# Performance work log

Measured on AMD Instinct MI355X. Metric: run time of the kernel, lower is better.

Reference implementation:

```python
import jax, jax.numpy as jnp
import numpy as np
import math

B, S, D, H = 2, 2048, 512, 8
DK = D // H  # 64
NEG_INF = float('-inf')


def setup_inputs() -> dict:
    key = jax.random.key(0)
    ks = jax.random.split(key, 16)
    s = 1.0 / math.sqrt(D)
    return {
        'in_Q': jax.random.normal(ks[0], (B, S, D), jnp.float32),
        'in_K': jax.random.normal(ks[1], (B, S, D), jnp.float32),
        'in_V': jax.random.normal(ks[2], (B, S, D), jnp.float32),
        'row_pad_mask': jax.random.randint(ks[3], (B, S), 0, 2, jnp.int32),
        'col_pad_mask': jax.random.randint(ks[4], (B, S), 0, 2, jnp.int32),
        'W_Q': jax.random.uniform(ks[5], (D, D), jnp.float32, -s, s),
        'b_Q': jax.random.uniform(ks[6], (D,), jnp.float32, -s, s),
        'W_K': jax.random.uniform(ks[7], (D, D), jnp.float32, -s, s),
        'b_K': jax.random.uniform(ks[8], (D,), jnp.float32, -s, s),
        'W_V': jax.random.uniform(ks[9], (D, D), jnp.float32, -s, s),
        'b_V': jax.random.uniform(ks[10], (D,), jnp.float32, -s, s),
        'W_O': jax.random.uniform(ks[11], (D, D), jnp.float32, -s, s),
        'b_O': jax.random.uniform(ks[12], (D,), jnp.float32, -s, s),
    }


def reference(in_Q, in_K, in_V, row_pad_mask, col_pad_mask,
              W_Q, b_Q, W_K, b_K, W_V, b_V, W_O, b_O):
    b, sq, _ = in_Q.shape
    sk = in_K.shape[1]
    # projections (torch Linear: x @ W.T + b)
    Q = in_Q @ W_Q.T + b_Q
    K = in_K @ W_K.T + b_K
    V = in_V @ W_V.T + b_V
    # chunk along feature dim + stack == reshape to heads: [b, h, s, dk]
    Qh = Q.reshape(b, sq, H, DK).transpose(0, 2, 1, 3)
    Kh = K.reshape(b, sk, H, DK).transpose(0, 2, 1, 3)
    Vh = V.reshape(b, sk, H, DK).transpose(0, 2, 1, 3)
    scores = jnp.einsum('bhqd,bhkd->bhqk', Qh, Kh) / math.sqrt(DK)
    # causal mask (additive -inf above diagonal, as in the original)
    causal = jnp.triu(jnp.full((sq, sk), NEG_INF, scores.dtype), k=1)
    scores = scores + causal
    # padding masks: pad masks encode lengths via their row sums
    row_len = row_pad_mask.sum(axis=1)  # [b]
    col_len = col_pad_mask.sum(axis=1)
    row_np = jnp.arange(sq)[None, :] < row_len[:, None]  # [b, sq]
    col_np = jnp.arange(sk)[None, :] < col_len[:, None]  # [b, sk]
    non_pad = (row_np[:, :, None] & col_np[:, None, :])[:, None]  # [b,1,sq,sk]
    scores = jnp.where(non_pad, scores, NEG_INF)
    p = jax.nn.softmax(scores, axis=-1)
    p = jnp.nan_to_num(p)  # fully-masked rows -> 0 (matches torch nan_to_num)
    attn = jnp.einsum('bhqk,bhkd->bhqd', p, Vh)
    Hcat = attn.transpose(0, 2, 1, 3).reshape(b, sq, D)
    return Hcat @ W_O.T + b_O
```

## Files before the change

kernel.cpp:

```cpp
#include <hip/hip_runtime.h>

#define S_LEN 2048
#define D_MODEL 512
#define NHEAD 8
#define BATCH 2

typedef __attribute__((ext_vector_type(8))) short bf16x8;
typedef __attribute__((ext_vector_type(4))) float f32x4;

__device__ __forceinline__ unsigned short f2bf(float f) {
    union { float f; unsigned u; } v; v.f = f;
    unsigned u = v.u + 0x7FFFu + ((v.u >> 16) & 1u);
    return (unsigned short)(u >> 16);
}

__device__ __forceinline__ void gl_lds16(const unsigned short* g, unsigned short* l) {
    __builtin_amdgcn_global_load_lds(
        (const __attribute__((address_space(1))) void*)g,
        (__attribute__((address_space(3))) void*)l,
        16, 0, 0);
}

__global__ __launch_bounds__(256) void cvtlens_kernel(
    const float* __restrict__ inQ, const float* __restrict__ inK, const float* __restrict__ inV,
    const float* __restrict__ WQ, const float* __restrict__ WK,
    const float* __restrict__ WV, const float* __restrict__ WO,
    const int* __restrict__ rpm, const int* __restrict__ cpm,
    unsigned short* __restrict__ Xbf, unsigned short* __restrict__ Wbf,
    int* __restrict__ lens)
{
    const int t = threadIdx.x;
    if (blockIdx.x < 2) {
        __shared__ int red[256];
        const int b = blockIdx.x;
        int sr = 0, sc2 = 0;
        for (int i = t; i < S_LEN; i += 256) {
            sr  += rpm[b * S_LEN + i];
            sc2 += cpm[b * S_LEN + i];
        }
        red[t] = sr;
        __syncthreads();
        for (int off = 128; off > 0; off >>= 1) {
            if (t < off) red[t] += red[t + off];
            __syncthreads();
        }
        if (t == 0) lens[b * 2 + 0] = red[0];
        __syncthreads();
        red[t] = sc2;
        __syncthreads();
        for (int off = 128; off > 0; off >>= 1) {
            if (t < off) red[t] += red[t + off];
            __syncthreads();
        }
        if (t == 0) lens[b * 2 + 1] = red[0];
    }

    const int NXC = 786432;
    const int NTOT = 917504;
    const int stride = gridDim.x * 256;
    for (int c = blockIdx.x * 256 + t; c < NTOT; c += stride) {
        if (c < NXC) {
            const int flat = c << 3;
            const int z = flat >> 21;
            const int off = flat & 2097151;
            const float* src = ((z == 0) ? inQ : (z == 1) ? inK : inV) + off;
            float4 a = *(const float4*)src;
            float4 d = *(const float4*)(src + 4);
            unsigned short* w = Xbf + flat;
            w[0] = f2bf(a.x); w[1] = f2bf(a.y); w[2] = f2bf(a.z); w[3] = f2bf(a.w);
            w[4] = f2bf(d.x); w[5] = f2bf(d.y); w[6] = f2bf(d.z); w[7] = f2bf(d.w);
        } else {
            const int wflat = (c - NXC) << 3;
            const int wz = wflat >> 18;
            const int off = wflat & 262143;
            const float* src = ((wz == 0) ? WQ : (wz == 1) ? WK : (wz == 2) ? WV : WO) + off;
            float4 a = *(const float4*)src;
            float4 d = *(const float4*)(src + 4);
            unsigned short* w = Wbf + wflat;
            w[0] = f2bf(a.x); w[1] = f2bf(a.y); w[2] = f2bf(a.z); w[3] = f2bf(a.w);
            w[4] = f2bf(d.x); w[5] = f2bf(d.y); w[6] = f2bf(d.z); w[7] = f2bf(d.w);
        }
    }
}

__global__ __launch_bounds__(256) void proj_gemm(
    const unsigned short* __restrict__ Xbf, const unsigned short* __restrict__ Wbf,
    const float* __restrict__ bQ, const float* __restrict__ bK, const float* __restrict__ bV,
    const int* __restrict__ lens,
    unsigned short* __restrict__ Qg, unsigned short* __restrict__ Kg,
    unsigned short* __restrict__ VTg)
{
    __shared__ __align__(16) unsigned short Xld[2][8192];
    __shared__ __align__(16) unsigned short Wld[2][8192];

    const int z = blockIdx.z;
    const int tileS = blockIdx.x * 128;
    const int tileF = blockIdx.y * 128;
    const int bb0 = tileS >> 11;
    const int rl = lens[bb0 * 2], cl = lens[bb0 * 2 + 1];
    const int limit = (z == 0) ? rl : cl;
    if ((tileS & 2047) >= limit) return;

    const unsigned short* X = Xbf + (size_t)z * (4096 * 512);
    const unsigned short* W = Wbf + (size_t)z * (512 * 512);
    const float* bias = (z == 0) ? bQ : (z == 1) ? bK : bV;

    const int t = threadIdx.x;
    const int wv = t >> 6, lane = t & 63, l15 = lane & 15, quad = lane >> 4;
    const int ro = lane >> 3;
    const int lc8 = ((lane & 7) ^ ro) * 8;

    const unsigned short* gX = X + (size_t)(tileS + wv * 32 + ro) * 512 + lc8;
    const unsigned short* gW = W + (size_t)(tileF + wv * 32 + ro) * 512 + lc8;
    const int wvo = wv * 2048;

    const int f_off = (wv & 1) * 64, s_off = (wv >> 1) * 64;
    const int swk = l15 & 7;

    f32x4 acc[4][4] = {};

    #pragma unroll
    for (int j = 0; j < 4; ++j) {
        gl_lds16(gX + j * 4096, &Xld[0][wvo + j * 512]);
        gl_lds16(gW + j * 4096, &Wld[0][wvo + j * 512]);
    }

    for (int kk = 0; kk < 8; ++kk) {
        __syncthreads();
        if (kk < 7) {
            const int k0 = (kk + 1) * 64;
            const int nb = (kk + 1) & 1;
            #pragma unroll
            for (int j = 0; j < 4; ++j) {
                gl_lds16(gX + k0 + j * 4096, &Xld[nb][wvo + j * 512]);
                gl_lds16(gW + k0 + j * 4096, &Wld[nb][wvo + j * 512]);
            }
        }
        const unsigned short* Xb = Xld[kk & 1];
        const unsigned short* Wb = Wld[kk & 1];
        #pragma unroll
        for (int kk2 = 0; kk2 < 2; ++kk2) {
            bf16x8 wf[4], xf[4];
            #pragma unroll
            for (int i = 0; i < 4; ++i) {
                const int rw = f_off + i * 16 + l15;
                wf[i] = *(const bf16x8*)(Wb + rw * 64 + ((kk2 * 4 + quad) ^ swk) * 8);
                const int rx = s_off + i * 16 + l15;
                xf[i] = *(const bf16x8*)(Xb + rx * 64 + ((kk2 * 4 + quad) ^ swk) * 8);
            }
            #pragma unroll
            for (int ft = 0; ft < 4; ++ft)
                #pragma unroll
                for (int st = 0; st < 4; ++st)
                    acc[ft][st] = __builtin_amdgcn_mfma_f32_16x16x32_bf16(
                        wf[ft], xf[st], acc[ft][st], 0, 0, 0);
        }
    }

    const float oscale = (z == 0) ? 0.125f : 1.0f;
    #pragma unroll
    for (int ft = 0; ft < 4; ++ft) {
        const int f = tileF + f_off + ft * 16 + quad * 4;
        const int h = f >> 6, dk = f & 63;
        const float b0 = bias[f], b1 = bias[f + 1], b2 = bias[f + 2], b3 = bias[f + 3];
        #pragma unroll
        for (int st = 0; st < 4; ++st) {
            const int s = tileS + s_off + st * 16 + l15;
            const int bb = s >> 11, seq = s & 2047;
            const f32x4 a = acc[ft][st];
            if (z <= 1) {
                unsigned short* dst = ((z == 0) ? Qg : Kg)
                    + ((size_t)((bb * 8 + h) * 2048 + seq)) * 64 + dk;
                ushort4 u;
                u.x = f2bf((a[0] + b0) * oscale); u.y = f2bf((a[1] + b1) * oscale);
                u.z = f2bf((a[2] + b2) * oscale); u.w = f2bf((a[3] + b3) * oscale);
                *(ushort4*)dst = u;
            } else {
                unsigned short* dst = VTg
                    + ((size_t)((bb * 8 + h) * 64 + dk)) * 2048 + seq;
                dst[0]    = f2bf(a[0] + b0);
                dst[2048] = f2bf(a[1] + b1);
                dst[4096] = f2bf(a[2] + b2);
                dst[6144] = f2bf(a[3] + b3);
            }
        }
    }
}

__global__ __launch_bounds__(256) void attn_kernel(
    const unsigned short* __restrict__ Qg, const unsigned short* __restrict__ Kg,
    const unsigned short* __restrict__ VTg, const int* __restrict__ lens,
    unsigned short* __restrict__ AO)
{
    __shared__ __align__(16) char smem[32768 + 9216 + 512];
    unsigned short* stage = (unsigned short*)smem;
    unsigned short* Plb   = (unsigned short*)(smem + 32768);
    float* Ml = (float*)(smem + 32768 + 9216);
    float* Ll = Ml + 64;

    const int t = threadIdx.x;
    const int wv = t >> 6, lane = t & 63, l15 = lane & 15, quad = lane >> 4;
    const int bh = blockIdx.y;
    const int b = bh >> 3, h = bh & 7;
    const int q0 = blockIdx.x * 16;
    const int rl = lens[b * 2], cl = lens[b * 2 + 1];

    if (q0 >= rl) {
        const int row = t >> 4, cg = t & 15;
        ushort4 zz = {0, 0, 0, 0};
        *(ushort4*)(AO + ((size_t)(b * 2048 + q0 + row)) * 512 + h * 64 + cg * 4) = zz;
        return;
    }

    const unsigned short* Qrow = Qg + ((size_t)(bh * 2048 + q0 + l15)) * 64;
    const bf16x8 aq0 = *(const bf16x8*)(Qrow + quad * 8);
    const bf16x8 aq1 = *(const bf16x8*)(Qrow + 32 + quad * 8);

    unsigned short* stw = stage + wv * 4096;
    unsigned short* pb  = Plb + wv * (16 * 72);

    const int sro = lane >> 3;
    const int sc8 = ((lane & 7) ^ sro) * 8;
    const int kg_off  = sro * 64 + sc8;
    const int vtg_off = sro * 2048 + sc8;
    const int sw7 = l15 & 7;

    f32x4 oacc[4] = {};
    float m_[4], l_[4];
    #pragma unroll
    for (int r = 0; r < 4; ++r) { m_[r] = -__builtin_inff(); l_[r] = 0.f; }

    const int q_end = q0 + 16;
    const int kv_max = (cl < q_end) ? cl : q_end;
    const int ntiles = (kv_max + 63) >> 6;
    const int qrow0 = q0 + quad * 4;

    for (int kt = wv; kt < ntiles; kt += 4) {
        const int kv0 = kt * 64;

        {
            const unsigned short* kg = Kg + ((size_t)(bh * 2048 + kv0)) * 64 + kg_off;
            #pragma unroll
            for (int j = 0; j < 8; ++j)
                gl_lds16(kg + j * 512, stw + j * 512);
        }
        __builtin_amdgcn_s_waitcnt(0x0070);

        f32x4 sc[4] = {};
        #pragma unroll
        for (int ct = 0; ct < 4; ++ct) {
            const unsigned short* krow = stw + (ct * 16 + l15) * 64;
            const bf16x8 kf0 = *(const bf16x8*)(krow + ((quad    ) ^ sw7) * 8);
            const bf16x8 kf1 = *(const bf16x8*)(krow + ((quad + 4) ^ sw7) * 8);
            sc[ct] = __builtin_amdgcn_mfma_f32_16x16x32_bf16(aq0, kf0, sc[ct], 0, 0, 0);
            sc[ct] = __builtin_amdgcn_mfma_f32_16x16x32_bf16(aq1, kf1, sc[ct], 0, 0, 0);
        }
        __builtin_amdgcn_s_waitcnt(0x0070);

        {
            const unsigned short* vg = VTg + ((size_t)(bh * 64)) * 2048 + kv0 + vtg_off;
            #pragma unroll
            for (int j = 0; j < 8; ++j)
                gl_lds16(vg + j * 16384, stw + j * 512);
        }

        const bool full = (kv0 + 64 <= q0) && (kv0 + 64 <= cl) && (q_end <= rl);

        #pragma unroll
        for (int r = 0; r < 4; ++r) {
            const int q = qrow0 + r;
            float mx = -__builtin_inff();
            if (full) {
                #pragma unroll
                for (int ct = 0; ct < 4; ++ct) mx = fmaxf(mx, sc[ct][r]);
            } else {
                #pragma unroll
                for (int ct = 0; ct < 4; ++ct) {
                    const int kv = kv0 + ct * 16 + l15;
                    float s = sc[ct][r];
                    const bool valid = (q < rl) && (kv < cl) && (kv <= q);
                    s = valid ? s : -__builtin_inff();
                    sc[ct][r] = s;
                    mx = fmaxf(mx, s);
                }
            }
            mx = fmaxf(mx, __shfl_xor(mx, 1, 16));
            mx = fmaxf(mx, __shfl_xor(mx, 2, 16));
            mx = fmaxf(mx, __shfl_xor(mx, 4, 16));
            mx = fmaxf(mx, __shfl_xor(mx, 8, 16));

            const float mold = m_[r];
            const float mnew = fmaxf(mold, mx);
            const float alpha = (mold == -__builtin_inff()) ? 0.f : __expf(mold - mnew);
            float psum = 0.f;
            #pragma unroll
            for (int ct = 0; ct < 4; ct++) {
                const float sv = sc[ct][r];
                const float p = (mnew == -__builtin_inff()) ? 0.f : __expf(sv - mnew);
                sc[ct][r] = p;
                psum += p;
            }
            psum += __shfl_xor(psum, 1, 16);
            psum += __shfl_xor(psum, 2, 16);
            psum += __shfl_xor(psum, 4, 16);
            psum += __shfl_xor(psum, 8, 16);
            l_[r] = alpha * l_[r] + psum;
            m_[r] = mnew;
            #pragma unroll
            for (int ct = 0; ct < 4; ct++) oacc[ct][r] *= alpha;
        }

        #pragma unroll
        for (int ct = 0; ct < 4; ++ct) {
            #pragma unroll
            for (int r = 0; r < 4; ++r)
                pb[(quad * 4 + r) * 72 + ct * 16 + l15] = f2bf(sc[ct][r]);
        }
        const bf16x8 pf0 = *(const bf16x8*)(pb + l15 * 72 + quad * 8);
        const bf16x8 pf1 = *(const bf16x8*)(pb + l15 * 72 + 32 + quad * 8);

        __builtin_amdgcn_s_waitcnt(0x0070);
        #pragma unroll
        for (int ct = 0; ct < 4; ++ct) {
            const unsigned short* vrow = stw + (ct * 16 + l15) * 64;
            const bf16x8 vf0 = *(const bf16x8*)(vrow + ((quad    ) ^ sw7) * 8);
            const bf16x8 vf1 = *(const bf16x8*)(vrow + ((quad + 4) ^ sw7) * 8);
            oacc[ct] = __builtin_amdgcn_mfma_f32_16x16x32_bf16(pf0, vf0, oacc[ct], 0, 0, 0);
            oacc[ct] = __builtin_amdgcn_mfma_f32_16x16x32_bf16(pf1, vf1, oacc[ct], 0, 0, 0);
        }
    }

    if (l15 == 0) {
        #pragma unroll
        for (int r = 0; r < 4; ++r) {
            Ml[wv * 16 + quad * 4 + r] = m_[r];
            Ll[wv * 16 + quad * 4 + r] = l_[r];
        }
    }
    __syncthreads();

    float* Po = (float*)smem;
    #pragma unroll
    for (int ct = 0; ct < 4; ++ct) {
        #pragma unroll
        for (int r = 0; r < 4; ++r)
            Po[wv * 1088 + (quad * 4 + r) * 68 + ct * 16 + l15] = oacc[ct][r];
    }
    __syncthreads();

    const int row = t >> 4, cg = t & 15;
    float mw[4];
    float mstar = -__builtin_inff();
    #pragma unroll
    for (int w = 0; w < 4; ++w) {
        mw[w] = Ml[w * 16 + row];
        mstar = fmaxf(mstar, mw[w]);
    }
    f32x4 o = {};
    if (mstar != -__builtin_inff()) {
        float lst = 0.f;
        #pragma unroll
        for (int w = 0; w < 4; ++w) {
            const float sw = (mw[w] == -__builtin_inff()) ? 0.f : __expf(mw[w] - mstar);
            lst += sw * Ll[w * 16 + row];
            const f32x4 pv = *(const f32x4*)&Po[w * 1088 + row * 68 + cg * 4];
            o[0] += sw * pv[0]; o[1] += sw * pv[1];
            o[2] += sw * pv[2]; o[3] += sw * pv[3];
        }
        const float inv = (lst > 0.f) ? 1.f / lst : 0.f;
        o[0] *= inv; o[1] *= inv; o[2] *= inv; o[3] *= inv;
    }
    ushort4 u;
    u.x = f2bf(o[0]); u.y = f2bf(o[1]); u.z = f2bf(o[2]); u.w = f2bf(o[3]);
    *(ushort4*)(AO + ((size_t)(b * 2048 + q0 + row)) * 512 + h * 64 + cg * 4) = u;
}

__global__ __launch_bounds__(256) void out_gemm(
    const unsigned short* __restrict__ AO, const unsigned short* __restrict__ Wbf,
    const float* __restrict__ bO, const int* __restrict__ lens, float* __restrict__ out)
{
    __shared__ __align__(16) unsigned short Xld[2][8192];
    __shared__ __align__(16) unsigned short Wld[2][8192];

    const int tileS = blockIdx.x * 128;
    const int tileF = blockIdx.y * 128;
    const int bb0 = tileS >> 11;
    const int rl = lens[bb0 * 2];
    const int t = threadIdx.x;

    if ((tileS & 2047) >= rl) {
        const int r0 = t >> 2;
        const int cg = (t & 3) * 32;
        float4 bv[8];
        #pragma unroll
        for (int j = 0; j < 8; ++j) bv[j] = *(const float4*)(bO + tileF + cg + j * 4);
        #pragma unroll
        for (int i = 0; i < 2; ++i) {
            float* orow = out + (size_t)(tileS + i * 64 + r0) * 512 + tileF + cg;
            #pragma unroll
            for (int j = 0; j < 8; ++j) *(float4*)(orow + j * 4) = bv[j];
        }
        return;
    }

    const unsigned short* W = Wbf + (size_t)3 * (512 * 512);
    const int wv = t >> 6, lane = t & 63, l15 = lane & 15, quad = lane >> 4;
    const int ro = lane >> 3;
    const int lc8 = ((lane & 7) ^ ro) * 8;

    const unsigned short* gX = AO + (size_t)(tileS + wv * 32 + ro) * 512 + lc8;
    const unsigned short* gW = W + (size_t)(tileF + wv * 32 + ro) * 512 + lc8;
    const int wvo = wv * 2048;

    const int f_off = (wv & 1) * 64, s_off = (wv >> 1) * 64;
    const int swk = l15 & 7;

    f32x4 acc[4][4] = {};

    #pragma unroll
    for (int j = 0; j < 4; ++j) {
        gl_lds16(gX + j * 4096, &Xld[0][wvo + j * 512]);
        gl_lds16(gW + j * 4096, &Wld[0][wvo + j * 512]);
    }

    for (int kk = 0; kk < 8; ++kk) {
        __syncthreads();
        if (kk < 7) {
            const int k0 = (kk + 1) * 64;
            const int nb = (kk + 1) & 1;
            #pragma unroll
            for (int j = 0; j < 4; ++j) {
                gl_lds16(gX + k0 + j * 4096, &Xld[nb][wvo + j * 512]);
                gl_lds16(gW + k0 + j * 4096, &Wld[nb][wvo + j * 512]);
            }
        }
        const unsigned short* Xb = Xld[kk & 1];
        const unsigned short* Wb = Wld[kk & 1];
        #pragma unroll
        for (int kk2 = 0; kk2 < 2; ++kk2) {
            bf16x8 wf[4], xf[4];
            #pragma unroll
            for (int i = 0; i < 4; ++i) {
                const int rw = f_off + i * 16 + l15;
                wf[i] = *(const bf16x8*)(Wb + rw * 64 + ((kk2 * 4 + quad) ^ swk) * 8);
                const int rx = s_off + i * 16 + l15;
                xf[i] = *(const bf16x8*)(Xb + rx * 64 + ((kk2 * 4 + quad) ^ swk) * 8);
            }
            #pragma unroll
            for (int ft = 0; ft < 4; ++ft)
                #pragma unroll
                for (int st = 0; st < 4; ++st)
                    acc[ft][st] = __builtin_amdgcn_mfma_f32_16x16x32_bf16(
                        wf[ft], xf[st], acc[ft][st], 0, 0, 0);
        }
    }

    #pragma unroll
    for (int ft = 0; ft < 4; ++ft) {
        const int f = tileF + f_off + ft * 16 + quad * 4;
        const float4 bv = *(const float4*)(bO + f);
        #pragma unroll
        for (int st = 0; st < 4; ++st) {
            const int s = tileS + s_off + st * 16 + l15;
            float4 o;
            o.x = acc[ft][st][0] + bv.x;
            o.y = acc[ft][st][1] + bv.y;
            o.z = acc[ft][st][2] + bv.z;
            o.w = acc[ft][st][3] + bv.w;
            *(float4*)(out + (size_t)s * 512 + f) = o;
        }
    }
}

extern "C" void kernel_launch(void* const* d_in, const int* in_sizes, int n_in,
                              void* d_out, int out_size, void* d_ws, size_t ws_size,
                              hipStream_t stream)
{
    const float* inQ = (const float*)d_in[0];
    const float* inK = (const float*)d_in[1];
    const float* inV = (const float*)d_in[2];
    const int*   rpm = (const int*)d_in[3];
    const int*   cpm = (const int*)d_in[4];
    const float* WQ  = (const float*)d_in[5];
    const float* bQ  = (const float*)d_in[6];
    const float* WK  = (const float*)d_in[7];
    const float* bK  = (const float*)d_in[8];
    const float* WV  = (const float*)d_in[9];
    const float* bV  = (const float*)d_in[10];
    const float* WO  = (const float*)d_in[11];
    const float* bO  = (const float*)d_in[12];
    float* out = (float*)d_out;

    char* ws = (char*)d_ws;
    unsigned short* Xbf = (unsigned short*)(ws);
    unsigned short* Wbf = (unsigned short*)(ws + 12582912);
    unsigned short* Qg  = (unsigned short*)(ws + 14680064);
    unsigned short* Kg  = (unsigned short*)(ws + 18874368);
    unsigned short* VTg = (unsigned short*)(ws + 23068672);
    unsigned short* AO  = (unsigned short*)(ws + 27262976);
    int* lens           = (int*)(ws + 31457280);

    cvtlens_kernel<<<dim3(1792), dim3(256), 0, stream>>>(
        inQ, inK, inV, WQ, WK, WV, WO, rpm, cpm, Xbf, Wbf, lens);
    proj_gemm<<<dim3(32, 4, 3), dim3(256), 0, stream>>>(
        Xbf, Wbf, bQ, bK, bV, lens, Qg, Kg, VTg);
    attn_kernel<<<dim3(128, 16), dim3(256), 0, stream>>>(Qg, Kg, VTg, lens, AO);
    out_gemm<<<dim3(32, 4), dim3(256), 0, stream>>>(AO, Wbf, bO, lens, out);
}
```

Before: 151.7 us.

## Fuse fp32-to-bf16 conversion into projection and output GEMMs, drop convert kernel

Removes the separate conversion kernel. The projection GEMM now loads fp32 inputs and weights straight into registers, converts them to bf16 and writes them to padded LDS. Its tile grows to 128x256 and it also computes the pad lengths. The output GEMM likewise converts W_O from fp32 on the fly. This saves one launch and the bf16 round trip through global memory. The costs are that the padded-length early exit in proj_gemm is gone, so fully padded tiles are now computed, and that the global_load_lds double buffering is replaced by register prefetch with two barriers per k-step.

Result: slower. 179.3 us (+18.2%).

```diff
diff --git a/kernel.cpp b/kernel.cpp
--- a/kernel.cpp
+++ b/kernel.cpp
@@ -12,6 +12,15 @@
     union { float f; unsigned u; } v; v.f = f;
     unsigned u = v.u + 0x7FFFu + ((v.u >> 16) & 1u);
     return (unsigned short)(u >> 16);
+}
+
+__device__ __forceinline__ bf16x8 pack8(float4 a, float4 b) {
+    bf16x8 r;
+    r[0] = (short)f2bf(a.x); r[1] = (short)f2bf(a.y);
+    r[2] = (short)f2bf(a.z); r[3] = (short)f2bf(a.w);
+    r[4] = (short)f2bf(b.x); r[5] = (short)f2bf(b.y);
+    r[6] = (short)f2bf(b.z); r[7] = (short)f2bf(b.w);
+    return r;
 }
 
 __device__ __forceinline__ void gl_lds16(const unsigned short* g, unsigned short* l) {
@@ -21,17 +30,24 @@
         16, 0, 0);
 }
 
-__global__ __launch_bounds__(256) void cvtlens_kernel(
+__global__ __launch_bounds__(256, 1) void proj_gemm(
     const float* __restrict__ inQ, const float* __restrict__ inK, const float* __restrict__ inV,
-    const float* __restrict__ WQ, const float* __restrict__ WK,
-    const float* __restrict__ WV, const float* __restrict__ WO,
-    const int* __restrict__ rpm, const int* __restrict__ cpm,
-    unsigned short* __restrict__ Xbf, unsigned short* __restrict__ Wbf,
-    int* __restrict__ lens)
+    const float* __restrict__ WQ,  const float* __restrict__ WK,  const float* __restrict__ WV,
+    const float* __restrict__ bQ,  const float* __restrict__ bK,  const float* __restrict__ bV,
+    const int* __restrict__ rpm,   const int* __restrict__ cpm,
+    unsigned short* __restrict__ Qg, unsigned short* __restrict__ Kg,
+    unsigned short* __restrict__ VTg, int* __restrict__ lens)
 {
+    __shared__ __align__(16) unsigned short XldP[128 * 76];
+    __shared__ __align__(16) unsigned short WldP[256 * 76];
+
+    const int z = blockIdx.z;
+    const int tileS = blockIdx.x * 128;
+    const int fh = blockIdx.y * 256;
     const int t = threadIdx.x;
-    if (blockIdx.x < 2) {
-        __shared__ int red[256];
+
+    if (blockIdx.x < 2 && blockIdx.y == 0 && z == 0) {
+        int* red = (int*)XldP;
         const int b = blockIdx.x;
         int sr = 0, sc2 = 0;
         for (int i = t; i < S_LEN; i += 256) {
@@ -55,119 +71,72 @@
         if (t == 0) lens[b * 2 + 1] = red[0];
     }
 
-    const int NXC = 786432;
-    const int NTOT = 917504;
-    const int stride = gridDim.x * 256;
-    for (int c = blockIdx.x * 256 + t; c < NTOT; c += stride) {
-        if (c < NXC) {
-            const int flat = c << 3;
-            const int z = flat >> 21;
-            const int off = flat & 2097151;
-            const float* src = ((z == 0) ? inQ : (z == 1) ? inK : inV) + off;
-            float4 a = *(const float4*)src;
-            float4 d = *(const float4*)(src + 4);
-            unsigned short* w = Xbf + flat;
-            w[0] = f2bf(a.x); w[1] = f2bf(a.y); w[2] = f2bf(a.z); w[3] = f2bf(a.w);
-            w[4] = f2bf(d.x); w[5] = f2bf(d.y); w[6] = f2bf(d.z); w[7] = f2bf(d.w);
-        } else {
-            const int wflat = (c - NXC) << 3;
-            const int wz = wflat >> 18;
-            const int off = wflat & 262143;
-            const float* src = ((wz == 0) ? WQ : (wz == 1) ? WK : (wz == 2) ? WV : WO) + off;
-            float4 a = *(const float4*)src;
-            float4 d = *(const float4*)(src + 4);
-            unsigned short* w = Wbf + wflat;
-            w[0] = f2bf(a.x); w[1] = f2bf(a.y); w[2] = f2bf(a.z); w[3] = f2bf(a.w);
-            w[4] = f2bf(d.x); w[5] = f2bf(d.y); w[6] = f2bf(d.z); w[7] = f2bf(d.w);
-        }
-    }
-}
-
-__global__ __launch_bounds__(256) void proj_gemm(
-    const unsigned short* __restrict__ Xbf, const unsigned short* __restrict__ Wbf,
-    const float* __restrict__ bQ, const float* __restrict__ bK, const float* __restrict__ bV,
-    const int* __restrict__ lens,
-    unsigned short* __restrict__ Qg, unsigned short* __restrict__ Kg,
-    unsigned short* __restrict__ VTg)
-{
-    __shared__ __align__(16) unsigned short Xld[2][8192];
-    __shared__ __align__(16) unsigned short Wld[2][8192];
-
-    const int z = blockIdx.z;
-    const int tileS = blockIdx.x * 128;
-    const int tileF = blockIdx.y * 128;
-    const int bb0 = tileS >> 11;
-    const int rl = lens[bb0 * 2], cl = lens[bb0 * 2 + 1];
-    const int limit = (z == 0) ? rl : cl;
-    if ((tileS & 2047) >= limit) return;
-
-    const unsigned short* X = Xbf + (size_t)z * (4096 * 512);
-    const unsigned short* W = Wbf + (size_t)z * (512 * 512);
-    const float* bias = (z == 0) ? bQ : (z == 1) ? bK : bV;
-
-    const int t = threadIdx.x;
+    const float* X    = (z == 0) ? inQ : (z == 1) ? inK : inV;
+    const float* W    = (z == 0) ? WQ  : (z == 1) ? WK  : WV;
+    const float* bias = (z == 0) ? bQ  : (z == 1) ? bK  : bV;
+
     const int wv = t >> 6, lane = t & 63, l15 = lane & 15, quad = lane >> 4;
-    const int ro = lane >> 3;
-    const int lc8 = ((lane & 7) ^ ro) * 8;
-
-    const unsigned short* gX = X + (size_t)(tileS + wv * 32 + ro) * 512 + lc8;
-    const unsigned short* gW = W + (size_t)(tileF + wv * 32 + ro) * 512 + lc8;
-    const int wvo = wv * 2048;
-
-    const int f_off = (wv & 1) * 64, s_off = (wv >> 1) * 64;
-    const int swk = l15 & 7;
-
-    f32x4 acc[4][4] = {};
-
-    #pragma unroll
-    for (int j = 0; j < 4; ++j) {
-        gl_lds16(gX + j * 4096, &Xld[0][wvo + j * 512]);
-        gl_lds16(gW + j * 4096, &Wld[0][wvo + j * 512]);
-    }
+
+    const int xrow = t >> 1, xcol = (t & 1) * 32;
+    const float* gX = X + (size_t)(tileS + xrow) * 512 + xcol;
+    const float* gW = W + (size_t)(fh + t) * 512;
+
+    float4 xr[8], wr[16];
+    #pragma unroll
+    for (int j = 0; j < 8; ++j)  xr[j] = *(const float4*)(gX + j * 4);
+    #pragma unroll
+    for (int j = 0; j < 16; ++j) wr[j] = *(const float4*)(gW + j * 4);
+
+    f32x4 acc[4][8] = {};
+
+    unsigned short* xd = XldP + xrow * 76 + xcol;
+    unsigned short* wd = WldP + t * 76;
 
     for (int kk = 0; kk < 8; ++kk) {
+        __syncthreads();
+        #pragma unroll
+        for (int j = 0; j < 4; ++j)
+            *(bf16x8*)(xd + j * 8) = pack8(xr[2 * j], xr[2 * j + 1]);
+        #pragma unroll
+        for (int j = 0; j < 8; ++j)
+            *(bf16x8*)(wd + j * 8) = pack8(wr[2 * j], wr[2 * j + 1]);
         __syncthreads();
         if (kk < 7) {
             const int k0 = (kk + 1) * 64;
-            const int nb = (kk + 1) & 1;
-            #pragma unroll
-            for (int j = 0; j < 4; ++j) {
-                gl_lds16(gX + k0 + j * 4096, &Xld[nb][wvo + j * 512]);
-                gl_lds16(gW + k0 + j * 4096, &Wld[nb][wvo + j * 512]);
-            }
-        }
-        const unsigned short* Xb = Xld[kk & 1];
-        const unsigned short* Wb = Wld[kk & 1];
+            #pragma unroll
+            for (int j = 0; j < 8; ++j)  xr[j] = *(const float4*)(gX + k0 + j * 4);
+            #pragma unroll
+            for (int j = 0; j < 16; ++j) wr[j] = *(const float4*)(gW + k0 + j * 4);
+        }
         #pragma unroll
         for (int kk2 = 0; kk2 < 2; ++kk2) {
-            bf16x8 wf[4], xf[4];
-            #pragma unroll
-            for (int i = 0; i < 4; ++i) {
-                const int rw = f_off + i * 16 + l15;
-                wf[i] = *(const bf16x8*)(Wb + rw * 64 + ((kk2 * 4 + quad) ^ swk) * 8);
-                const int rx = s_off + i * 16 + l15;
-                xf[i] = *(const bf16x8*)(Xb + rx * 64 + ((kk2 * 4 + quad) ^ swk) * 8);
-            }
-            #pragma unroll
-            for (int ft = 0; ft < 4; ++ft)
+            bf16x8 wf[4], xf[8];
+            #pragma unroll
+            for (int i = 0; i < 4; ++i)
+                wf[i] = *(const bf16x8*)(WldP + (wv * 64 + i * 16 + l15) * 76 + kk2 * 32 + quad * 8);
+            #pragma unroll
+            for (int st = 0; st < 8; ++st)
+                xf[st] = *(const bf16x8*)(XldP + (st * 16 + l15) * 76 + kk2 * 32 + quad * 8);
+            #pragma unroll
+            for (int i = 0; i < 4; ++i)
                 #pragma unroll
-                for (int st = 0; st < 4; ++st)
-                    acc[ft][st] = __builtin_amdgcn_mfma_f32_16x16x32_bf16(
-                        wf[ft], xf[st], acc[ft][st], 0, 0, 0);
+                for (int st = 0; st < 8; ++st)
+                    acc[i][st] = __builtin_amdgcn_mfma_f32_16x16x32_bf16(
+                        wf[i], xf[st], acc[i][st], 0, 0, 0);
         }
     }
 
     const float oscale = (z == 0) ? 0.125f : 1.0f;
     #pragma unroll
-    for (int ft = 0; ft < 4; ++ft) {
-        const int f = tileF + f_off + ft * 16 + quad * 4;
+    for (int i = 0; i < 4; ++i) {
+        const int f = fh + wv * 64 + i * 16 + quad * 4;
         const int h = f >> 6, dk = f & 63;
         const float b0 = bias[f], b1 = bias[f + 1], b2 = bias[f + 2], b3 = bias[f + 3];
         #pragma unroll
-        for (int st = 0; st < 4; ++st) {
-            const int s = tileS + s_off + st * 16 + l15;
+        for (int st = 0; st < 8; ++st) {
+            const int s = tileS + st * 16 + l15;
             const int bb = s >> 11, seq = s & 2047;
-            const f32x4 a = acc[ft][st];
+            const f32x4 a = acc[i][st];
             if (z <= 1) {
                 unsigned short* dst = ((z == 0) ? Qg : Kg)
                     + ((size_t)((bb * 8 + h) * 2048 + seq)) * 64 + dk;
@@ -376,11 +345,11 @@
 }
 
 __global__ __launch_bounds__(256) void out_gemm(
-    const unsigned short* __restrict__ AO, const unsigned short* __restrict__ Wbf,
+    const unsigned short* __restrict__ AO, const float* __restrict__ WO,
     const float* __restrict__ bO, const int* __restrict__ lens, float* __restrict__ out)
 {
     __shared__ __align__(16) unsigned short Xld[2][8192];
-    __shared__ __align__(16) unsigned short Wld[2][8192];
+    __shared__ __align__(16) unsigned short WldP[128 * 76];
 
     const int tileS = blockIdx.x * 128;
     const int tileF = blockIdx.y * 128;
@@ -403,46 +372,51 @@
         return;
     }
 
-    const unsigned short* W = Wbf + (size_t)3 * (512 * 512);
     const int wv = t >> 6, lane = t & 63, l15 = lane & 15, quad = lane >> 4;
     const int ro = lane >> 3;
     const int lc8 = ((lane & 7) ^ ro) * 8;
 
     const unsigned short* gX = AO + (size_t)(tileS + wv * 32 + ro) * 512 + lc8;
-    const unsigned short* gW = W + (size_t)(tileF + wv * 32 + ro) * 512 + lc8;
     const int wvo = wv * 2048;
+
+    const int wrow = t >> 1, wcol = (t & 1) * 32;
+    const float* gWf = WO + (size_t)(tileF + wrow) * 512 + wcol;
+    unsigned short* wd = WldP + wrow * 76 + wcol;
 
     const int f_off = (wv & 1) * 64, s_off = (wv >> 1) * 64;
     const int swk = l15 & 7;
 
     f32x4 acc[4][4] = {};
-
-    #pragma unroll
-    for (int j = 0; j < 4; ++j) {
+    float4 wr[8];
+
+    #pragma unroll
+    for (int j = 0; j < 4; ++j)
         gl_lds16(gX + j * 4096, &Xld[0][wvo + j * 512]);
-        gl_lds16(gW + j * 4096, &Wld[0][wvo + j * 512]);
-    }
+    #pragma unroll
+    for (int j = 0; j < 8; ++j) wr[j] = *(const float4*)(gWf + j * 4);
 
     for (int kk = 0; kk < 8; ++kk) {
+        __syncthreads();
+        #pragma unroll
+        for (int j = 0; j < 4; ++j)
+            *(bf16x8*)(wd + j * 8) = pack8(wr[2 * j], wr[2 * j + 1]);
         __syncthreads();
         if (kk < 7) {
             const int k0 = (kk + 1) * 64;
             const int nb = (kk + 1) & 1;
             #pragma unroll
-            for (int j = 0; j < 4; ++j) {
+            for (int j = 0; j < 4; ++j)
                 gl_lds16(gX + k0 + j * 4096, &Xld[nb][wvo + j * 512]);
-                gl_lds16(gW + k0 + j * 4096, &Wld[nb][wvo + j * 512]);
-            }
+            #pragma unroll
+            for (int j = 0; j < 8; ++j) wr[j] = *(const float4*)(gWf + k0 + j * 4);
         }
         const unsigned short* Xb = Xld[kk & 1];
-        const unsigned short* Wb = Wld[kk & 1];
         #pragma unroll
         for (int kk2 = 0; kk2 < 2; ++kk2) {
             bf16x8 wf[4], xf[4];
             #pragma unroll
             for (int i = 0; i < 4; ++i) {
-                const int rw = f_off + i * 16 + l15;
-                wf[i] = *(const bf16x8*)(Wb + rw * 64 + ((kk2 * 4 + quad) ^ swk) * 8);
+                wf[i] = *(const bf16x8*)(WldP + (f_off + i * 16 + l15) * 76 + kk2 * 32 + quad * 8);
                 const int rx = s_off + i * 16 + l15;
                 xf[i] = *(const bf16x8*)(Xb + rx * 64 + ((kk2 * 4 + quad) ^ swk) * 8);
             }
@@ -492,18 +466,14 @@
     float* out = (float*)d_out;
 
     char* ws = (char*)d_ws;
-    unsigned short* Xbf = (unsigned short*)(ws);
-    unsigned short* Wbf = (unsigned short*)(ws + 12582912);
-    unsigned short* Qg  = (unsigned short*)(ws + 14680064);
-    unsigned short* Kg  = (unsigned short*)(ws + 18874368);
-    unsigned short* VTg = (unsigned short*)(ws + 23068672);
-    unsigned short* AO  = (unsigned short*)(ws + 27262976);
-    int* lens           = (int*)(ws + 31457280);
-
-    cvtlens_kernel<<<dim3(1792), dim3(256), 0, stream>>>(
-        inQ, inK, inV, WQ, WK, WV, WO, rpm, cpm, Xbf, Wbf, lens);
-    proj_gemm<<<dim3(32, 4, 3), dim3(256), 0, stream>>>(
-        Xbf, Wbf, bQ, bK, bV, lens, Qg, Kg, VTg);
+    unsigned short* Qg  = (unsigned short*)(ws);
+    unsigned short* Kg  = (unsigned short*)(ws + 4194304);
+    unsigned short* VTg = (unsigned short*)(ws + 8388608);
+    unsigned short* AO  = (unsigned short*)(ws + 12582912);
+    int* lens           = (int*)(ws + 16777216);
+
+    proj_gemm<<<dim3(32, 2, 3), dim3(256), 0, stream>>>(
+        inQ, inK, inV, WQ, WK, WV, bQ, bK, bV, rpm, cpm, Qg, Kg, VTg, lens);
     attn_kernel<<<dim3(128, 16), dim3(256), 0, stream>>>(Qg, Kg, VTg, lens, AO);
-    out_gemm<<<dim3(32, 4), dim3(256), 0, stream>>>(AO, Wbf, bO, lens, out);
-}
+    out_gemm<<<dim3(32, 4), dim3(256), 0, stream>>>(AO, WO, bO, lens, out);
+}
```
